# Kernel optimization log

Hardware: AMD Instinct MI355X
Metric: run time of the kernel (lower is better)

Reference implementation:

```python
import jax, jax.numpy as jnp
import numpy as np

N = 100000
E = 1600000
IN = 128
HID = 128
OUT = 64


def sage_conv(x, src, dst, deg_inv, W_l, b_l, W_r):
    # PyG SAGEConv (mean aggr): out = lin_l(mean_{j in N(i)} x_j) + lin_r(x_i)
    msgs = x[src]                                   # [E, F] gather
    agg = jax.ops.segment_sum(msgs, dst, num_segments=N)  # [N, F]
    agg = agg * deg_inv[:, None]                    # mean
    return agg @ W_l + b_l + x @ W_r


def setup_inputs() -> dict:
    key = jax.random.key(0)
    ks = jax.random.split(key, 9)
    x = jax.random.normal(ks[0], (N, IN), dtype=jnp.float32)
    edge_index = jax.random.randint(ks[1], (2, E), 0, N, dtype=jnp.int64)
    s = 1.0 / np.sqrt(IN)
    W1l = jax.random.uniform(ks[2], (IN, HID), jnp.float32, -s, s)
    b1 = jax.random.uniform(ks[3], (HID,), jnp.float32, -s, s)
    W1r = jax.random.uniform(ks[4], (IN, HID), jnp.float32, -s, s)
    s2 = 1.0 / np.sqrt(HID)
    W2l = jax.random.uniform(ks[5], (HID, HID), jnp.float32, -s2, s2)
    b2 = jax.random.uniform(ks[6], (HID,), jnp.float32, -s2, s2)
    W2r = jax.random.uniform(ks[7], (HID, HID), jnp.float32, -s2, s2)
    kl1, kl2 = jax.random.split(ks[8])
    Wlin = jax.random.uniform(kl1, (HID, OUT), jnp.float32, -s2, s2)
    blin = jax.random.uniform(kl2, (OUT,), jnp.float32, -s2, s2)
    return {"x": x, "edge_index": edge_index, "W1l": W1l, "b1": b1, "W1r": W1r,
            "W2l": W2l, "b2": b2, "W2r": W2r, "Wlin": Wlin, "blin": blin}


def reference(x, edge_index, W1l, b1, W1r, W2l, b2, W2r, Wlin, blin):
    src, dst = edge_index[0], edge_index[1]
    deg = jax.ops.segment_sum(jnp.ones((E,), jnp.float32), dst, num_segments=N)
    deg_inv = 1.0 / jnp.maximum(deg, 1.0)
    h = sage_conv(x, src, dst, deg_inv, W1l, b1, W1r)
    h = jax.nn.relu(h)
    # dropout: training=False -> identity
    h2 = sage_conv(h, src, dst, deg_inv, W2l, b2, W2r)
    h = jax.nn.relu(h + h2)
    return h @ Wlin + blin
```

## Files before the change

### kernel.cpp

```cpp
#include <hip/hip_runtime.h>
#include <hip/hip_bf16.h>
#include <cstdint>

#define NND 100000
#define NED 1600000
#define FIN 128
#define FOUT 64

typedef __bf16 bf16x8 __attribute__((ext_vector_type(8)));
typedef float f32x4 __attribute__((ext_vector_type(4)));

static __device__ inline unsigned short f2bf(float f) {
    unsigned int u = __builtin_bit_cast(unsigned int, f);
    unsigned int r = (u + 0x7fffu + ((u >> 16) & 1u)) >> 16;
    return (unsigned short)r;
}
static __device__ inline float bflo(unsigned int v) {
    return __builtin_bit_cast(float, v << 16);
}
static __device__ inline float bfhi(unsigned int v) {
    return __builtin_bit_cast(float, v & 0xffff0000u);
}
static __device__ inline float bf1(unsigned short u) {
    return __builtin_bit_cast(float, (unsigned int)u << 16);
}

__global__ __launch_bounds__(256) void k_deg_cast(const int* __restrict__ dst,
                                                  int* __restrict__ deg,
                                                  int* __restrict__ rank, int e,
                                                  const float* __restrict__ x,
                                                  unsigned int* __restrict__ xb,
                                                  int total2) {
    int i = blockIdx.x * 256 + threadIdx.x;
    if (i < e) rank[i] = atomicAdd(&deg[dst[i]], 1);
    if (i < total2) {
        float2 v = ((const float2*)x)[i];
        xb[i] = (unsigned int)f2bf(v.x) | ((unsigned int)f2bf(v.y) << 16);
    }
}

__global__ __launch_bounds__(1024) void k_scan1(const int* __restrict__ deg,
                                                int* __restrict__ psum, int n) {
    __shared__ int red[1024];
    int tid = threadIdx.x;
    int i = blockIdx.x * 1024 + tid;
    red[tid] = (i < n) ? deg[i] : 0;
    __syncthreads();
#pragma unroll
    for (int off = 512; off > 0; off >>= 1) {
        if (tid < off) red[tid] += red[tid + off];
        __syncthreads();
    }
    if (tid == 0) psum[blockIdx.x] = red[0];
}

__global__ __launch_bounds__(128) void k_scan2(int* __restrict__ psum, int nb) {
    int tid = threadIdx.x;
    int d = (tid < nb) ? psum[tid] : 0;
    int v = d;
#pragma unroll
    for (int off = 1; off < 64; off <<= 1) {
        int u = __shfl_up(v, off, 64);
        if ((tid & 63) >= off) v += u;
    }
    __shared__ int ws[2];
    if ((tid & 63) == 63) ws[tid >> 6] = v;
    __syncthreads();
    int base = (tid >= 64) ? ws[0] : 0;
    if (tid < nb) psum[tid] = base + v - d;
}

__global__ __launch_bounds__(1024) void k_scan3(const int* __restrict__ deg,
                                                const int* __restrict__ psum,
                                                int* __restrict__ offs,
                                                float* __restrict__ dinv,
                                                int n, int e) {
    int tid = threadIdx.x;
    int i = blockIdx.x * 1024 + tid;
    int d = (i < n) ? deg[i] : 0;
    int v = d;
#pragma unroll
    for (int off = 1; off < 64; off <<= 1) {
        int u = __shfl_up(v, off, 64);
        if ((tid & 63) >= off) v += u;
    }
    __shared__ int wsum[16];
    int wid = tid >> 6;
    if ((tid & 63) == 63) wsum[wid] = v;
    __syncthreads();
    if (tid < 16) {
        int w = wsum[tid];
#pragma unroll
        for (int off = 1; off < 16; off <<= 1) {
            int u = __shfl_up(w, off, 64);
            if (tid >= off) w += u;
        }
        wsum[tid] = w;
    }
    __syncthreads();
    int base = psum[blockIdx.x] + (wid ? wsum[wid - 1] : 0);
    if (i < n) {
        offs[i] = base + v - d;
        dinv[i] = 1.0f / fmaxf((float)d, 1.0f);
    }
    if (i == 0) offs[n] = e;
}

__global__ __launch_bounds__(256) void k_csr(const int* __restrict__ src,
                                             const int* __restrict__ dst,
                                             const int* __restrict__ rank,
                                             const int* __restrict__ offs,
                                             int* __restrict__ csr, int e) {
    int i = blockIdx.x * 256 + threadIdx.x;
    if (i < e) {
        csr[offs[dst[i]] + rank[i]] = src[i];
    }
}

static __device__ inline void pack_one(const float* __restrict__ W,
                                       unsigned short* __restrict__ out,
                                       int NTtot, int c_local, int nt,
                                       int chunkOff, int ncols, int lane) {
    int k = c_local * 32 + (lane >> 4) * 8;
    int n = nt * 16 + (lane & 15);
    unsigned short t[8];
#pragma unroll
    for (int j = 0; j < 8; j++) t[j] = f2bf(W[(size_t)(k + j) * ncols + n]);
    uint4 u;
    u.x = t[0] | ((unsigned)t[1] << 16);
    u.y = t[2] | ((unsigned)t[3] << 16);
    u.z = t[4] | ((unsigned)t[5] << 16);
    u.w = t[6] | ((unsigned)t[7] << 16);
    *(uint4*)&out[((size_t)((c_local + chunkOff) * NTtot + nt) * 64 + lane) * 8] = u;
}

__global__ __launch_bounds__(64) void k_packAll(const float* W1l, const float* W1r,
                                                const float* W2l, const float* W2r,
                                                const float* Wlin,
                                                unsigned short* p1, unsigned short* p2,
                                                unsigned short* ph) {
    int b = blockIdx.x, lane = threadIdx.x;
    if (b < 32)       pack_one(W1l, p1, 8, b >> 3, b & 7, 0, 128, lane);
    else if (b < 64)  { b -= 32; pack_one(W1r, p1, 8, b >> 3, b & 7, 4, 128, lane); }
    else if (b < 96)  { b -= 64; pack_one(W2l, p2, 8, b >> 3, b & 7, 0, 128, lane); }
    else if (b < 128) { b -= 96; pack_one(W2r, p2, 8, b >> 3, b & 7, 4, 128, lane); }
    else              { b -= 128; pack_one(Wlin, ph, 4, b >> 2, b & 3, 0, 64, lane); }
}

__global__ __launch_bounds__(256) void k_aggb(const uint4* __restrict__ feat4,
                                              const int* __restrict__ offs,
                                              const int* __restrict__ csr,
                                              const float* __restrict__ dinv,
                                              uint4* __restrict__ out4, int n) {
    int node = blockIdx.x * 4 + (threadIdx.x >> 6);
    if (node >= n) return;
    int lane = threadIdx.x & 63;
    int grp = lane >> 4;
    int ch = lane & 15;
    int beg = offs[node], end = offs[node + 1];

    float acc[8];
#pragma unroll
    for (int j = 0; j < 8; j++) acc[j] = 0.f;

    for (int i = beg; i < end; i += 8) {
        int e0 = i + grp;
        int e1 = i + 4 + grp;
        bool p0 = e0 < end, p1 = e1 < end;
        int s0 = p0 ? csr[e0] : 0;
        int s1 = p1 ? csr[e1] : 0;
        uint4 v0 = feat4[(size_t)s0 * 16 + ch];
        uint4 v1 = feat4[(size_t)s1 * 16 + ch];
        if (p0) {
            acc[0] += bflo(v0.x); acc[1] += bfhi(v0.x);
            acc[2] += bflo(v0.y); acc[3] += bfhi(v0.y);
            acc[4] += bflo(v0.z); acc[5] += bfhi(v0.z);
            acc[6] += bflo(v0.w); acc[7] += bfhi(v0.w);
        }
        if (p1) {
            acc[0] += bflo(v1.x); acc[1] += bfhi(v1.x);
            acc[2] += bflo(v1.y); acc[3] += bfhi(v1.y);
            acc[4] += bflo(v1.z); acc[5] += bfhi(v1.z);
            acc[6] += bflo(v1.w); acc[7] += bfhi(v1.w);
        }
    }
#pragma unroll
    for (int j = 0; j < 8; j++) {
        acc[j] += __shfl_xor(acc[j], 16);
        acc[j] += __shfl_xor(acc[j], 32);
    }
    if (grp == 0) {
        float di = dinv[node];
        uint4 o;
        o.x = (unsigned)f2bf(acc[0] * di) | ((unsigned)f2bf(acc[1] * di) << 16);
        o.y = (unsigned)f2bf(acc[2] * di) | ((unsigned)f2bf(acc[3] * di) << 16);
        o.z = (unsigned)f2bf(acc[4] * di) | ((unsigned)f2bf(acc[5] * di) << 16);
        o.w = (unsigned)f2bf(acc[6] * di) | ((unsigned)f2bf(acc[7] * di) << 16);
        out4[(size_t)node * 16 + ch] = o;
    }
}

template <int NT, int KCH, bool TWO, bool RELU, bool RESID, bool OUTBF>
__global__ __launch_bounds__(256) void k_mfma(const unsigned short* __restrict__ P,
                                              const unsigned short* __restrict__ Q,
                                              const unsigned short* __restrict__ Wp,
                                              const float* __restrict__ bias,
                                              const unsigned short* __restrict__ resid,
                                              void* __restrict__ outv, int n) {
    const int lane = threadIdx.x & 63;
    const int wave = threadIdx.x >> 6;
    const int quad = lane >> 4;
    const int row0 = blockIdx.x * 64 + wave * 16;
    int rowA = row0 + (lane & 15);
    if (rowA >= n) rowA = n - 1;

    f32x4 acc[NT];
#pragma unroll
    for (int t = 0; t < NT; t++) acc[t] = (f32x4){0.f, 0.f, 0.f, 0.f};

#pragma unroll
    for (int c = 0; c < KCH; c++) {
        const unsigned short* Abase = (TWO && c >= KCH / 2) ? Q : P;
        const int kk = (TWO ? (c & (KCH / 2 - 1)) : c) * 32 + quad * 8;
        bf16x8 a = *(const bf16x8*)&Abase[(size_t)rowA * 128 + kk];
#pragma unroll
        for (int t = 0; t < NT; t++) {
            bf16x8 b = *(const bf16x8*)&Wp[(size_t)((c * NT + t) * 64 + lane) * 8];
            acc[t] = __builtin_amdgcn_mfma_f32_16x16x32_bf16(a, b, acc[t], 0, 0, 0);
        }
    }

    const int col = lane & 15;
#pragma unroll
    for (int t = 0; t < NT; t++) {
        float bv = bias[t * 16 + col];
#pragma unroll
        for (int r = 0; r < 4; r++) {
            int row = row0 + quad * 4 + r;
            if (row < n) {
                float v = acc[t][r] + bv;
                if (RESID) v += bf1(resid[(size_t)row * 128 + t * 16 + col]);
                if (RELU) v = fmaxf(v, 0.f);
                if (OUTBF)
                    ((unsigned short*)outv)[(size_t)row * (NT * 16) + t * 16 + col] = f2bf(v);
                else
                    ((float*)outv)[(size_t)row * (NT * 16) + t * 16 + col] = v;
            }
        }
    }
}

extern "C" void kernel_launch(void* const* d_in, const int* in_sizes, int n_in,
                              void* d_out, int out_size, void* d_ws, size_t ws_size,
                              hipStream_t stream) {
    const float* x    = (const float*)d_in[0];
    const int*   ei   = (const int*)d_in[1];
    const float* W1l  = (const float*)d_in[2];
    const float* b1   = (const float*)d_in[3];
    const float* W1r  = (const float*)d_in[4];
    const float* W2l  = (const float*)d_in[5];
    const float* b2   = (const float*)d_in[6];
    const float* W2r  = (const float*)d_in[7];
    const float* Wlin = (const float*)d_in[8];
    const float* blin = (const float*)d_in[9];
    float* out = (float*)d_out;

    const int N = NND, E = NED;
    const int* src = ei;
    const int* dst = ei + E;
    const int NB = (N + 1023) / 1024;

    char* w = (char*)d_ws;
    int*   deg    = (int*)w;               w += (size_t)N * 4;
    int*   offs   = (int*)w;               w += (size_t)(N + 4) * 4;
    float* dinv   = (float*)w;             w += (size_t)N * 4;
    int*   psum   = (int*)w;               w += (size_t)((NB + 3) & ~3) * 4;
    int*   rank   = (int*)w;               w += (size_t)E * 4;
    int*   csr    = (int*)w;               w += (size_t)E * 4;
    unsigned short* p1  = (unsigned short*)w;  w += 256 * 128 * 2;
    unsigned short* p2  = (unsigned short*)w;  w += 256 * 128 * 2;
    unsigned short* ph  = (unsigned short*)w;  w += 128 * 64 * 2;
    unsigned short* xb  = (unsigned short*)w;  w += (size_t)N * 128 * 2;
    unsigned short* agg = (unsigned short*)w;  w += (size_t)N * 128 * 2;
    unsigned short* h1  = (unsigned short*)w;  w += (size_t)N * 128 * 2;
    unsigned short* h2  = (unsigned short*)w;  w += (size_t)N * 128 * 2;

    hipMemsetAsync(deg, 0, (size_t)N * 4, stream);

    k_deg_cast<<<(N * 64 + 255) / 256, 256, 0, stream>>>(dst, deg, rank, E, x,
                                                         (unsigned int*)xb, N * 64);
    k_scan1<<<NB, 1024, 0, stream>>>(deg, psum, N);
    k_scan2<<<1, 128, 0, stream>>>(psum, NB);
    k_scan3<<<NB, 1024, 0, stream>>>(deg, psum, offs, dinv, N, E);
    k_csr<<<E / 256, 256, 0, stream>>>(src, dst, rank, offs, csr, E);
    k_packAll<<<144, 64, 0, stream>>>(W1l, W1r, W2l, W2r, Wlin, p1, p2, ph);

    k_aggb<<<(N + 3) / 4, 256, 0, stream>>>((const uint4*)xb, offs, csr, dinv,
                                            (uint4*)agg, N);
    k_mfma<8, 8, true, true, false, true><<<(N + 63) / 64, 256, 0, stream>>>(
        agg, xb, p1, b1, nullptr, h1, N);

    k_aggb<<<(N + 3) / 4, 256, 0, stream>>>((const uint4*)h1, offs, csr, dinv,
                                            (uint4*)agg, N);
    k_mfma<8, 8, true, true, true, true><<<(N + 63) / 64, 256, 0, stream>>>(
        agg, h1, p2, b2, h1, h2, N);

    k_mfma<4, 4, false, false, false, false><<<(N + 63) / 64, 256, 0, stream>>>(
        h2, nullptr, ph, blin, nullptr, out, N);
}
```

Baseline: 470.7 us.

## Fuse output linear head into second SAGE GEMM and unroll gather loop

The final Linear layer is folded into the epilogue of the second SAGE MFMA kernel. The post-residual ReLU tile is staged through shared memory as bf16 and multiplied by the packed head weights in the same kernel, which removes the h2 intermediate buffer and one kernel launch. The neighbour aggregation loop now processes 16 edges per iteration with unpredicated loads, followed by a predicated tail, to raise memory-level parallelism. The cost is extra LDS use and register pressure in the fused kernel.

```diff
diff --git a/kernel.cpp b/kernel.cpp
--- a/kernel.cpp
+++ b/kernel.cpp
@@ -147,6 +147,12 @@
     else              { b -= 128; pack_one(Wlin, ph, 4, b >> 2, b & 3, 0, 64, lane); }
 }
 
+#define ACC8(v) do { \
+    acc[0].x += bflo((v).x); acc[0].y += bfhi((v).x); \
+    acc[1].x += bflo((v).y); acc[1].y += bfhi((v).y); \
+    acc[2].x += bflo((v).z); acc[2].y += bfhi((v).z); \
+    acc[3].x += bflo((v).w); acc[3].y += bfhi((v).w); } while (0)
+
 __global__ __launch_bounds__(256) void k_aggb(const uint4* __restrict__ feat4,
                                               const int* __restrict__ offs,
                                               const int* __restrict__ csr,
@@ -158,54 +164,61 @@
     int grp = lane >> 4;
     int ch = lane & 15;
     int beg = offs[node], end = offs[node + 1];
-
-    float acc[8];
-#pragma unroll
-    for (int j = 0; j < 8; j++) acc[j] = 0.f;
-
-    for (int i = beg; i < end; i += 8) {
-        int e0 = i + grp;
-        int e1 = i + 4 + grp;
-        bool p0 = e0 < end, p1 = e1 < end;
-        int s0 = p0 ? csr[e0] : 0;
-        int s1 = p1 ? csr[e1] : 0;
+    int deg = end - beg;
+
+    float2 acc[4];
+#pragma unroll
+    for (int j = 0; j < 4; j++) acc[j] = make_float2(0.f, 0.f);
+
+    int i = beg;
+    int fullEnd = beg + (deg & ~15);
+    for (; i < fullEnd; i += 16) {
+        int s0 = csr[i + grp];
+        int s1 = csr[i + 4 + grp];
+        int s2 = csr[i + 8 + grp];
+        int s3 = csr[i + 12 + grp];
         uint4 v0 = feat4[(size_t)s0 * 16 + ch];
         uint4 v1 = feat4[(size_t)s1 * 16 + ch];
-        if (p0) {
-            acc[0] += bflo(v0.x); acc[1] += bfhi(v0.x);
-            acc[2] += bflo(v0.y); acc[3] += bfhi(v0.y);
-            acc[4] += bflo(v0.z); acc[5] += bfhi(v0.z);
-            acc[6] += bflo(v0.w); acc[7] += bfhi(v0.w);
-        }
-        if (p1) {
-            acc[0] += bflo(v1.x); acc[1] += bfhi(v1.x);
-            acc[2] += bflo(v1.y); acc[3] += bfhi(v1.y);
-            acc[4] += bflo(v1.z); acc[5] += bfhi(v1.z);
-            acc[6] += bflo(v1.w); acc[7] += bfhi(v1.w);
-        }
-    }
-#pragma unroll
-    for (int j = 0; j < 8; j++) {
-        acc[j] += __shfl_xor(acc[j], 16);
-        acc[j] += __shfl_xor(acc[j], 32);
+        uint4 v2 = feat4[(size_t)s2 * 16 + ch];
+        uint4 v3 = feat4[(size_t)s3 * 16 + ch];
+        ACC8(v0); ACC8(v1); ACC8(v2); ACC8(v3);
+    }
+    if (i < end) {
+#pragma unroll
+        for (int g = 0; g < 4; g++) {
+            int e = i + g * 4 + grp;
+            bool p = e < end;
+            int s = csr[p ? e : beg];
+            uint4 v = feat4[(size_t)s * 16 + ch];
+            if (p) { ACC8(v); }
+        }
+    }
+#pragma unroll
+    for (int j = 0; j < 4; j++) {
+        acc[j].x += __shfl_xor(acc[j].x, 16);
+        acc[j].y += __shfl_xor(acc[j].y, 16);
+        acc[j].x += __shfl_xor(acc[j].x, 32);
+        acc[j].y += __shfl_xor(acc[j].y, 32);
     }
     if (grp == 0) {
         float di = dinv[node];
         uint4 o;
-        o.x = (unsigned)f2bf(acc[0] * di) | ((unsigned)f2bf(acc[1] * di) << 16);
-        o.y = (unsigned)f2bf(acc[2] * di) | ((unsigned)f2bf(acc[3] * di) << 16);
-        o.z = (unsigned)f2bf(acc[4] * di) | ((unsigned)f2bf(acc[5] * di) << 16);
-        o.w = (unsigned)f2bf(acc[6] * di) | ((unsigned)f2bf(acc[7] * di) << 16);
+        o.x = (unsigned)f2bf(acc[0].x * di) | ((unsigned)f2bf(acc[0].y * di) << 16);
+        o.y = (unsigned)f2bf(acc[1].x * di) | ((unsigned)f2bf(acc[1].y * di) << 16);
+        o.z = (unsigned)f2bf(acc[2].x * di) | ((unsigned)f2bf(acc[2].y * di) << 16);
+        o.w = (unsigned)f2bf(acc[3].x * di) | ((unsigned)f2bf(acc[3].y * di) << 16);
         out4[(size_t)node * 16 + ch] = o;
     }
 }
 
-template <int NT, int KCH, bool TWO, bool RELU, bool RESID, bool OUTBF>
+template <int NT, int KCH, bool TWO, bool RELU, bool RESID, bool HEAD, bool OUTBF>
 __global__ __launch_bounds__(256) void k_mfma(const unsigned short* __restrict__ P,
                                               const unsigned short* __restrict__ Q,
                                               const unsigned short* __restrict__ Wp,
                                               const float* __restrict__ bias,
                                               const unsigned short* __restrict__ resid,
+                                              const unsigned short* __restrict__ Wp2,
+                                              const float* __restrict__ bias2,
                                               void* __restrict__ outv, int n) {
     const int lane = threadIdx.x & 63;
     const int wave = threadIdx.x >> 6;
@@ -231,20 +244,59 @@
     }
 
     const int col = lane & 15;
-#pragma unroll
-    for (int t = 0; t < NT; t++) {
-        float bv = bias[t * 16 + col];
-#pragma unroll
-        for (int r = 0; r < 4; r++) {
-            int row = row0 + quad * 4 + r;
-            if (row < n) {
+    if (!HEAD) {
+#pragma unroll
+        for (int t = 0; t < NT; t++) {
+            float bv = bias[t * 16 + col];
+#pragma unroll
+            for (int r = 0; r < 4; r++) {
+                int row = row0 + quad * 4 + r;
+                if (row < n) {
+                    float v = acc[t][r] + bv;
+                    if (RESID) v += bf1(resid[(size_t)row * 128 + t * 16 + col]);
+                    if (RELU) v = fmaxf(v, 0.f);
+                    if (OUTBF)
+                        ((unsigned short*)outv)[(size_t)row * (NT * 16) + t * 16 + col] = f2bf(v);
+                    else
+                        ((float*)outv)[(size_t)row * (NT * 16) + t * 16 + col] = v;
+                }
+            }
+        }
+    } else {
+        __shared__ __align__(16) unsigned short sT[4][16 * 136];
+#pragma unroll
+        for (int t = 0; t < NT; t++) {
+            float bv = bias[t * 16 + col];
+#pragma unroll
+            for (int r = 0; r < 4; r++) {
+                int row = row0 + quad * 4 + r;
+                int rr = row < n ? row : n - 1;
                 float v = acc[t][r] + bv;
-                if (RESID) v += bf1(resid[(size_t)row * 128 + t * 16 + col]);
+                if (RESID) v += bf1(resid[(size_t)rr * 128 + t * 16 + col]);
                 if (RELU) v = fmaxf(v, 0.f);
-                if (OUTBF)
-                    ((unsigned short*)outv)[(size_t)row * (NT * 16) + t * 16 + col] = f2bf(v);
-                else
-                    ((float*)outv)[(size_t)row * (NT * 16) + t * 16 + col] = v;
+                sT[wave][(quad * 4 + r) * 136 + t * 16 + col] = f2bf(v);
+            }
+        }
+        f32x4 hacc[4];
+#pragma unroll
+        for (int t = 0; t < 4; t++) hacc[t] = (f32x4){0.f, 0.f, 0.f, 0.f};
+#pragma unroll
+        for (int c = 0; c < 4; c++) {
+            bf16x8 a = *(const bf16x8*)&sT[wave][(lane & 15) * 136 + c * 32 + quad * 8];
+#pragma unroll
+            for (int t = 0; t < 4; t++) {
+                bf16x8 b = *(const bf16x8*)&Wp2[(size_t)((c * 4 + t) * 64 + lane) * 8];
+                hacc[t] = __builtin_amdgcn_mfma_f32_16x16x32_bf16(a, b, hacc[t], 0, 0, 0);
+            }
+        }
+#pragma unroll
+        for (int t = 0; t < 4; t++) {
+            float bv = bias2[t * 16 + col];
+#pragma unroll
+            for (int r = 0; r < 4; r++) {
+                int row = row0 + quad * 4 + r;
+                if (row < n)
+                    ((float*)outv)[(size_t)row * 64 + t * 16 + col] = hacc[t][r] + bv;
             }
         }
     }
@@ -283,7 +335,6 @@
     unsigned short* xb  = (unsigned short*)w;  w += (size_t)N * 128 * 2;
     unsigned short* agg = (unsigned short*)w;  w += (size_t)N * 128 * 2;
     unsigned short* h1  = (unsigned short*)w;  w += (size_t)N * 128 * 2;
-    unsigned short* h2  = (unsigned short*)w;  w += (size_t)N * 128 * 2;
 
     hipMemsetAsync(deg, 0, (size_t)N * 4, stream);
 
@@ -297,14 +348,11 @@
 
     k_aggb<<<(N + 3) / 4, 256, 0, stream>>>((const uint4*)xb, offs, csr, dinv,
                                             (uint4*)agg, N);
-    k_mfma<8, 8, true, true, false, true><<<(N + 63) / 64, 256, 0, stream>>>(
-        agg, xb, p1, b1, nullptr, h1, N);
+    k_mfma<8, 8, true, true, false, false, true><<<(N + 63) / 64, 256, 0, stream>>>(
+        agg, xb, p1, b1, nullptr, nullptr, nullptr, h1, N);
 
     k_aggb<<<(N + 3) / 4, 256, 0, stream>>>((const uint4*)h1, offs, csr, dinv,
                                             (uint4*)agg, N);
-    k_mfma<8, 8, true, true, true, true><<<(N + 63) / 64, 256, 0, stream>>>(
-        agg, h1, p2, b2, h1, h2, N);
-
-    k_mfma<4, 4, false, false, false, false><<<(N + 63) / 64, 256, 0, stream>>>(
-        h2, nullptr, ph, blin, nullptr, out, N);
-}
+    k_mfma<8, 8, true, true, true, true, false><<<(N + 63) / 64, 256, 0, stream>>>(
+        agg, h1, p2, b2, h1, ph, blin, out, N);
+}
```

New measurement: 443.8 us. 1.06x faster.
